# Performance work log

Hardware: AMD Instinct MI355X
Metric: run time of the kernel (lower is better)

The kernel has to match this reference:

```python
import jax, jax.numpy as jnp
import numpy as np
from jax.scipy.linalg import solve_triangular

LOAD = 1e-5       # diagonal loading used by solve_loaded / GEVD stabilization
EPS_DENOM = 1e-6  # clamp in compute_mvdr_bf
REF_MIC = 0


def _covariances(masks, X):
    # masks: (B, S, 3, F, N) real, X: (B, C, F, N) complex
    # returns three (B, S, F, C, C) Hermitian covariance stacks
    return [jnp.einsum('bsfn,bcfn,bdfn->bsfcd', masks[:, :, i], X, jnp.conj(X))
            for i in range(3)]


def _gevd_rtf(A, B):
    # Generalized eigh A v = lam B v via Cholesky whitening; take eigvec of
    # largest eigenvalue, normalize by reference mic (compute_mvdr_rtf_eigh).
    d = A.shape[-1]
    eye = jnp.eye(d, dtype=A.dtype)
    L = jnp.linalg.cholesky(B + LOAD * eye)          # (..., C, C) lower
    T = solve_triangular(L, A, lower=True)           # L^{-1} A
    C = solve_triangular(L, jnp.conj(jnp.swapaxes(T, -1, -2)), lower=True)
    C = jnp.conj(jnp.swapaxes(C, -1, -2))            # L^{-1} A L^{-H}
    C = 0.5 * (C + jnp.conj(jnp.swapaxes(C, -1, -2)))  # enforce Hermitian
    _, u = jnp.linalg.eigh(C)                        # ascending eigenvalues
    u_max = u[..., :, -1]                            # dominant whitened eigvec
    Lh = jnp.conj(jnp.swapaxes(L, -1, -2))
    v = solve_triangular(Lh, u_max[..., None], lower=False)[..., 0]  # L^{-H} u
    return v / v[..., REF_MIC:REF_MIC + 1]


def _mvdr_weights(R_noise, rtf):
    # compute_mvdr_bf: a = (R + load*I)^{-1} rtf ; w = a / max(re(rtf^H a), eps)
    d = R_noise.shape[-1]
    eye = jnp.eye(d, dtype=R_noise.dtype)
    a = jnp.linalg.solve(R_noise + LOAD * eye, rtf[..., None])[..., 0]
    denom = jnp.real(jnp.einsum('...c,...c->...', jnp.conj(rtf), a))
    denom = jnp.maximum(denom, EPS_DENOM)
    return a / denom[..., None]


def setup_inputs() -> dict:
    key = jax.random.key(0)
    k1, k2, k3 = jax.random.split(key, 3)
    B, S, C, F, N = 4, 2, 6, 512, 2000
    return {
        'X_re': jax.random.normal(k1, (B, C, F, N), jnp.float32),
        'X_im': jax.random.normal(k2, (B, C, F, N), jnp.float32),
        'masks': jax.random.uniform(k3, (B, S, 3, F, N), jnp.float32),
    }


def reference(X_re, X_im, masks):
    X = jax.lax.complex(X_re, X_im)                  # (B, C, F, N)
    R_tgt, R_noise_1, R_noise_2 = _covariances(masks, X)
    rtf = _gevd_rtf(R_tgt, R_noise_2)                # (B, S, F, C)
    bf = _mvdr_weights(R_noise_1, rtf)               # (B, S, F, C)
    Y = jnp.einsum('bcfn,bsfc->bsfn', X, jnp.conj(bf))
    # return real/imag stacked to keep harness dtypes real
    return jnp.stack((Y.real, Y.imag), axis=-1)      # (B, S, F, N, 2)
```

## Files before the change

### kernel.cpp

```cpp
#include <hip/hip_runtime.h>

#define B_ 4
#define S_ 2
#define C_ 6
#define F_ 512
#define N_ 2000
#define CH_ (F_ * N_)
#define LOAD_CONST 1e-5
#define EPS_DENOM_ 1e-6
#define NV4 (N_ / 4)
#define NCHUNK 8

__device__ __forceinline__ void gld_lds16(const void* gp, void* lp) {
  __builtin_amdgcn_global_load_lds(
      (const __attribute__((address_space(1))) unsigned int*)gp,
      (__attribute__((address_space(3))) unsigned int*)lp, 16, 0, 0);
}

__global__ __launch_bounds__(64, 2) void cov_kernel(
    const float* __restrict__ Xre, const float* __restrict__ Xim,
    const float* __restrict__ masks, float* __restrict__ cov) {
  __shared__ float sh[2][14][256];

  const int nwg = B_ * F_ * 3;
  const int cpx = nwg / 8;
  const int Bh = blockIdx.x;
  const int l = (Bh & 7) * cpx + (Bh >> 3);
  const int bf = l / 3;
  const int i = l - bf * 3;
  const int b = bf / F_;
  const int f = bf - b * F_;
  const int lane = threadIdx.x;

  const size_t xb = (size_t)b * C_ * CH_ + (size_t)f * N_;

  const float4* gbase[14];
#pragma unroll
  for (int st = 0; st < 12; ++st) {
    const float* p = (st < 6) ? (Xre + xb + (size_t)st * CH_)
                              : (Xim + xb + (size_t)(st - 6) * CH_);
    gbase[st] = (const float4*)p;
  }
  gbase[12] = (const float4*)(masks + ((size_t)b * 6 + i) * CH_ + (size_t)f * N_);
  gbase[13] = (const float4*)(masks + ((size_t)b * 6 + 3 + i) * CH_ + (size_t)f * N_);

  auto stage = [&](int bb, int ch) {
    int idx = ch * 64 + lane;
    if (idx >= NV4) idx = NV4 - 1;
#pragma unroll
    for (int st = 0; st < 14; ++st)
      gld_lds16(gbase[st] + idx, &sh[bb][st][0]);
  };

  float acc0d[6] = {}, acc0r[15] = {}, acc0i[15] = {};
  float acc1d[6] = {}, acc1r[15] = {}, acc1i[15] = {};

  stage(0, 0);
  stage(1, 1);

  for (int ch = 0; ch < NCHUNK; ++ch) {
    const int bb = ch & 1;

    if (ch < NCHUNK - 1) {
      asm volatile("s_waitcnt vmcnt(14)" ::: "memory");
    } else {
      asm volatile("s_waitcnt vmcnt(0)" ::: "memory");
    }

#pragma unroll
    for (int e = 0; e < 4; ++e) {
      const int fo = lane + 64 * e;
      float xre[6], xie[6];
#pragma unroll
      for (int c = 0; c < 6; ++c) {
        xre[c] = sh[bb][c][fo];
        xie[c] = sh[bb][6 + c][fo];
      }
      float m0 = sh[bb][12][fo];
      float m1 = sh[bb][13][fo];
      if (ch * 256 + fo >= N_) { m0 = 0.f; m1 = 0.f; }

#pragma unroll
      for (int c = 0; c < 6; ++c) {
        const float d = fmaf(xre[c], xre[c], xie[c] * xie[c]);
        acc0d[c] = fmaf(m0, d, acc0d[c]);
        acc1d[c] = fmaf(m1, d, acc1d[c]);
      }
      int p = 0;
#pragma unroll
      for (int c = 0; c < 6; ++c) {
#pragma unroll
        for (int d2 = c + 1; d2 < 6; ++d2) {
          const float pr = fmaf(xre[c], xre[d2], xie[c] * xie[d2]);
          const float pi = fmaf(xie[c], xre[d2], -(xre[c] * xie[d2]));
          acc0r[p] = fmaf(m0, pr, acc0r[p]);
          acc0i[p] = fmaf(m0, pi, acc0i[p]);
          acc1r[p] = fmaf(m1, pr, acc1r[p]);
          acc1i[p] = fmaf(m1, pi, acc1i[p]);
          ++p;
        }
      }
    }

    asm volatile("s_waitcnt lgkmcnt(0)" ::: "memory");
    if (ch + 2 < NCHUNK) stage(bb, ch + 2);
  }

#pragma unroll
  for (int c = 0; c < 6; ++c) {
#pragma unroll
    for (int o = 32; o > 0; o >>= 1) {
      acc0d[c] += __shfl_xor(acc0d[c], o, 64);
      acc1d[c] += __shfl_xor(acc1d[c], o, 64);
    }
  }
#pragma unroll
  for (int p2 = 0; p2 < 15; ++p2) {
#pragma unroll
    for (int o = 32; o > 0; o >>= 1) {
      acc0r[p2] += __shfl_xor(acc0r[p2], o, 64);
      acc0i[p2] += __shfl_xor(acc0i[p2], o, 64);
      acc1r[p2] += __shfl_xor(acc1r[p2], o, 64);
      acc1i[p2] += __shfl_xor(acc1i[p2], o, 64);
    }
  }

  if (lane == 0) {
    float* o0 = cov + ((size_t)bf * 6 + i) * 36;
    float* o1 = cov + ((size_t)bf * 6 + 3 + i) * 36;
#pragma unroll
    for (int c = 0; c < 6; ++c) { o0[c] = acc0d[c]; o1[c] = acc1d[c]; }
#pragma unroll
    for (int p2 = 0; p2 < 15; ++p2) {
      o0[6 + 2 * p2] = acc0r[p2];  o0[7 + 2 * p2] = acc0i[p2];
      o1[6 + 2 * p2] = acc1r[p2];  o1[7 + 2 * p2] = acc1i[p2];
    }
  }
}

__device__ __forceinline__ void load_herm(const float* __restrict__ p,
                                          double* mr, double* mi) {
#pragma unroll
  for (int c = 0; c < 6; ++c) { mr[c * 6 + c] = (double)p[c]; mi[c * 6 + c] = 0.0; }
#pragma unroll
  for (int c = 0; c < 6; ++c) {
#pragma unroll
    for (int d = c + 1; d < 6; ++d) {
      const int pidx = 6 + 2 * ((11 - c) * c / 2 + (d - c - 1));
      double re = (double)p[pidx];
      double im = (double)p[pidx + 1];
      mr[c * 6 + d] = re;  mi[c * 6 + d] = im;
      mr[d * 6 + c] = re;  mi[d * 6 + c] = -im;
    }
  }
}

__device__ __forceinline__ void chol6(double* mr, double* mi) {
#pragma unroll
  for (int k = 0; k < 6; ++k) {
    double d = mr[k * 6 + k];
#pragma unroll
    for (int j = 0; j < 6; ++j) {
      if (j < k) d -= mr[k * 6 + j] * mr[k * 6 + j] + mi[k * 6 + j] * mi[k * 6 + j];
    }
    d = sqrt(fmax(d, 1e-300));
    mr[k * 6 + k] = d;  mi[k * 6 + k] = 0.0;
    double inv = 1.0 / d;
#pragma unroll
    for (int r = k + 1; r < 6; ++r) {
      double xre = mr[r * 6 + k], xim = mi[r * 6 + k];
#pragma unroll
      for (int j = 0; j < 6; ++j) {
        if (j < k) {
          double ar = mr[r * 6 + j], ai = mi[r * 6 + j];
          double br = mr[k * 6 + j], bi = mi[k * 6 + j];
          xre -= ar * br + ai * bi;
          xim -= ai * br - ar * bi;
        }
      }
      mr[r * 6 + k] = xre * inv;  mi[r * 6 + k] = xim * inv;
    }
  }
}

__device__ __forceinline__ void chol_solve(const double* mr, const double* mi,
                                           double* xr, double* xi) {
  double yr[6], yi[6];
#pragma unroll
  for (int r = 0; r < 6; ++r) {
    double tr = xr[r], ti = xi[r];
#pragma unroll
    for (int k = 0; k < 6; ++k) {
      if (k < r) {
        double ar = mr[r * 6 + k], ai = mi[r * 6 + k];
        tr -= ar * yr[k] - ai * yi[k];
        ti -= ar * yi[k] + ai * yr[k];
      }
    }
    double inv = 1.0 / mr[r * 6 + r];
    yr[r] = tr * inv;  yi[r] = ti * inv;
  }
#pragma unroll
  for (int r = 5; r >= 0; --r) {
    double tr = yr[r], ti = yi[r];
#pragma unroll
    for (int k = 5; k >= 0; --k) {
      if (k > r) {
        double ar = mr[k * 6 + r], ai = -mi[k * 6 + r];
        tr -= ar * xr[k] - ai * xi[k];
        ti -= ar * xi[k] + ai * xr[k];
      }
    }
    double inv = 1.0 / mr[r * 6 + r];
    xr[r] = tr * inv;  xi[r] = ti * inv;
  }
}

__global__ __launch_bounds__(64, 1) void solve_kernel(
    const float* __restrict__ cov, float* __restrict__ wts) {
  const int t = blockIdx.x * 64 + threadIdx.x;
  if (t >= B_ * S_ * F_) return;
  const int f = t % F_;
  const int s = (t / F_) % S_;
  const int b = t / (F_ * S_);
  const float* cb = cov + (((size_t)(b * F_ + f)) * 6 + s * 3) * 36;

  double Lr[36], Li[36];
  load_herm(cb + 72, Lr, Li);
#pragma unroll
  for (int k = 0; k < 6; ++k) Lr[k * 6 + k] += LOAD_CONST;
  chol6(Lr, Li);

  double Ar[36], Ai[36];
  load_herm(cb, Ar, Ai);

  double Cr[36], Ci[36];
#pragma unroll
  for (int k = 0; k < 36; ++k) { Cr[k] = 0.0; Ci[k] = 0.0; }
#pragma unroll
  for (int j = 0; j < 6; ++j) {
    double yr[6], yi[6];
#pragma unroll
    for (int r = 5; r >= 0; --r) {
      double tr = (r == j) ? 1.0 : 0.0, ti = 0.0;
#pragma unroll
      for (int k = 5; k >= 0; --k) {
        if (k > r) {
          double ar = Lr[k * 6 + r], ai = -Li[k * 6 + r];
          tr -= ar * yr[k] - ai * yi[k];
          ti -= ar * yi[k] + ai * yr[k];
        }
      }
      double inv = 1.0 / Lr[r * 6 + r];
      yr[r] = tr * inv;  yi[r] = ti * inv;
    }
    double zr[6], zi[6];
#pragma unroll
    for (int r = 0; r < 6; ++r) {
      double tr = 0, ti = 0;
#pragma unroll
      for (int k = 0; k < 6; ++k) {
        double ar = Ar[r * 6 + k], ai = Ai[r * 6 + k];
        tr += ar * yr[k] - ai * yi[k];
        ti += ar * yi[k] + ai * yr[k];
      }
      zr[r] = tr;  zi[r] = ti;
    }
    double cr[6], ci2[6];
#pragma unroll
    for (int r = 0; r < 6; ++r) {
      double tr = zr[r], ti = zi[r];
#pragma unroll
      for (int k = 0; k < 6; ++k) {
        if (k < r) {
          double ar = Lr[r * 6 + k], ai = Li[r * 6 + k];
          tr -= ar * cr[k] - ai * ci2[k];
          ti -= ar * ci2[k] + ai * cr[k];
        }
      }
      double inv = 1.0 / Lr[r * 6 + r];
      cr[r] = tr * inv;  ci2[r] = ti * inv;
    }
#pragma unroll
    for (int r = 0; r < 6; ++r) {
      if (r < j)       { Cr[r * 6 + j] += 0.5 * cr[r];  Ci[r * 6 + j] += 0.5 * ci2[r]; }
      else if (r == j) { Cr[r * 6 + r] += cr[r]; }
      else             { Cr[j * 6 + r] += 0.5 * cr[r];  Ci[j * 6 + r] -= 0.5 * ci2[r]; }
    }
  }

  double Gr[36], Gi[36];
#pragma unroll
  for (int k = 0; k < 36; ++k) { Gr[k] = Cr[k]; Gi[k] = Ci[k]; }

#pragma unroll
  for (int sweep = 0; sweep < 8; ++sweep) {
#pragma unroll
    for (int p = 0; p < 5; ++p) {
#pragma unroll
      for (int q = p + 1; q < 6; ++q) {
        double gr = Cr[p * 6 + q], gi = Ci[p * 6 + q];
        double g2 = gr * gr + gi * gi;
        if (g2 > 1e-26) {
          double g = sqrt(g2);
          double wr = gr / g, wi = -gi / g;
          double alpha = Cr[p * 6 + p], beta = Cr[q * 6 + q];
          double tau = (beta - alpha) / (2.0 * g);
          double tt = (tau >= 0.0 ? 1.0 : -1.0) / (fabs(tau) + sqrt(1.0 + tau * tau));
          double cc = 1.0 / sqrt(1.0 + tt * tt);
          double ss = tt * cc;
#pragma unroll
          for (int r = 0; r < 6; ++r) {
            if (r == p || r == q) continue;
            double rpr = (r < p) ? Cr[r * 6 + p] : Cr[p * 6 + r];
            double rpi = (r < p) ? Ci[r * 6 + p] : -Ci[p * 6 + r];
            double rqr = (r < q) ? Cr[r * 6 + q] : Cr[q * 6 + r];
            double rqi = (r < q) ? Ci[r * 6 + q] : -Ci[q * 6 + r];
            double wqr = wr * rqr - wi * rqi;
            double wqi = wr * rqi + wi * rqr;
            double nrpr = cc * rpr - ss * wqr;
            double nrpi = cc * rpi - ss * wqi;
            double nrqr = ss * rpr + cc * wqr;
            double nrqi = ss * rpi + cc * wqi;
            if (r < p) { Cr[r * 6 + p] = nrpr;  Ci[r * 6 + p] = nrpi; }
            else       { Cr[p * 6 + r] = nrpr;  Ci[p * 6 + r] = -nrpi; }
            if (r < q) { Cr[r * 6 + q] = nrqr;  Ci[r * 6 + q] = nrqi; }
            else       { Cr[q * 6 + r] = nrqr;  Ci[q * 6 + r] = -nrqi; }
          }
          Cr[p * 6 + p] = alpha - tt * g;
          Cr[q * 6 + q] = beta + tt * g;
          Cr[p * 6 + q] = 0.0;  Ci[p * 6 + q] = 0.0;
        }
      }
    }
  }

  double lmax = Cr[0];
  lmax = fmax(lmax, Cr[7]);  lmax = fmax(lmax, Cr[14]);
  lmax = fmax(lmax, Cr[21]); lmax = fmax(lmax, Cr[28]);
  lmax = fmax(lmax, Cr[35]);

  double Mr[36], Mi[36];
  double shift = lmax + fmax(1e-8 * fabs(lmax), 1e-30);
#pragma unroll
  for (int r = 0; r < 6; ++r) {
#pragma unroll
    for (int c = 0; c < 6; ++c) {
      double gre, gim;
      if (r == c)     { gre = Gr[r * 6 + c]; gim = 0.0; }
      else if (r < c) { gre = Gr[r * 6 + c]; gim = Gi[r * 6 + c]; }
      else            { gre = Gr[c * 6 + r]; gim = -Gi[c * 6 + r]; }
      Mr[r * 6 + c] = (r == c) ? (shift - gre) : -gre;
      Mi[r * 6 + c] = -gim;
    }
  }
  chol6(Mr, Mi);

  double ur[6] = {1.0, 0.8, -0.6, 1.1, -0.3, 0.5};
  double ui[6] = {0.2, -0.9, 0.7, 0.1, 1.0, -0.4};
#pragma unroll
  for (int it = 0; it < 2; ++it) {
    chol_solve(Mr, Mi, ur, ui);
    double nn = 0;
#pragma unroll
    for (int r = 0; r < 6; ++r) nn += ur[r] * ur[r] + ui[r] * ui[r];
    double innv = 1.0 / sqrt(fmax(nn, 1e-300));
#pragma unroll
    for (int r = 0; r < 6; ++r) { ur[r] *= innv; ui[r] *= innv; }
  }

  double vr[6], vi[6];
#pragma unroll
  for (int r = 5; r >= 0; --r) {
    double tr = ur[r], ti = ui[r];
#pragma unroll
    for (int k = 5; k >= 0; --k) {
      if (k > r) {
        double ar = Lr[k * 6 + r], ai = -Li[k * 6 + r];
        tr -= ar * vr[k] - ai * vi[k];
        ti -= ar * vi[k] + ai * vr[k];
      }
    }
    double inv = 1.0 / Lr[r * 6 + r];
    vr[r] = tr * inv;  vi[r] = ti * inv;
  }

  double id2 = 1.0 / (vr[0] * vr[0] + vi[0] * vi[0]);
  double rtr[6], rti[6];
#pragma unroll
  for (int r = 0; r < 6; ++r) {
    rtr[r] = (vr[r] * vr[0] + vi[r] * vi[0]) * id2;
    rti[r] = (vi[r] * vr[0] - vr[r] * vi[0]) * id2;
  }

  load_herm(cb + 36, Mr, Mi);
#pragma unroll
  for (int k = 0; k < 6; ++k) Mr[k * 6 + k] += LOAD_CONST;
  chol6(Mr, Mi);
  double ar2[6], ai2[6];
#pragma unroll
  for (int r = 0; r < 6; ++r) { ar2[r] = rtr[r]; ai2[r] = rti[r]; }
  chol_solve(Mr, Mi, ar2, ai2);

  double denom = 0;
#pragma unroll
  for (int r = 0; r < 6; ++r) denom += rtr[r] * ar2[r] + rti[r] * ai2[r];
  denom = fmax(denom, EPS_DENOM_);
  double idn = 1.0 / denom;

  float* wp = wts + (size_t)t * 12;
#pragma unroll
  for (int c = 0; c < 6; ++c) {
    wp[2 * c]     = (float)(ar2[c] * idn);
    wp[2 * c + 1] = (float)(-ai2[c] * idn);
  }
}

__global__ __launch_bounds__(256) void bf_kernel(
    const float* __restrict__ Xre, const float* __restrict__ Xim,
    const float* __restrict__ wts, float* __restrict__ out) {
  const int blk = blockIdx.x;
  const int b = blk / F_;
  const int f = blk - b * F_;
  const size_t xb = (size_t)b * C_ * CH_ + (size_t)f * N_;

  float wr[2][6], wi[2][6];
#pragma unroll
  for (int s = 0; s < 2; ++s) {
    const float* wp = wts + (((size_t)(b * S_ + s)) * F_ + f) * 12;
#pragma unroll
    for (int c = 0; c < 6; ++c) { wr[s][c] = wp[2 * c]; wi[s][c] = wp[2 * c + 1]; }
  }
  float4* o0 = (float4*)(out + ((size_t)(b * S_ + 0) * F_ + f) * N_ * 2);
  float4* o1 = (float4*)(out + ((size_t)(b * S_ + 1) * F_ + f) * N_ * 2);

  const int NV = N_ / 4;
  for (int n4 = threadIdx.x; n4 < NV; n4 += 256) {
    float4 xr[6], xi[6];
#pragma unroll
    for (int c = 0; c < 6; ++c) {
      xr[c] = ((const float4*)(Xre + xb + (size_t)c * CH_))[n4];
      xi[c] = ((const float4*)(Xim + xb + (size_t)c * CH_))[n4];
    }
#pragma unroll
    for (int s = 0; s < 2; ++s) {
      float yrx = 0.f, yix = 0.f, yry = 0.f, yiy = 0.f;
      float yrz = 0.f, yiz = 0.f, yrw = 0.f, yiw = 0.f;
#pragma unroll
      for (int c = 0; c < 6; ++c) {
        const float WR = wr[s][c], WI = wi[s][c];
        yrx = fmaf(xr[c].x, WR, fmaf(-xi[c].x, WI, yrx));
        yix = fmaf(xr[c].x, WI, fmaf(xi[c].x, WR, yix));
        yry = fmaf(xr[c].y, WR, fmaf(-xi[c].y, WI, yry));
        yiy = fmaf(xr[c].y, WI, fmaf(xi[c].y, WR, yiy));
        yrz = fmaf(xr[c].z, WR, fmaf(-xi[c].z, WI, yrz));
        yiz = fmaf(xr[c].z, WI, fmaf(xi[c].z, WR, yiz));
        yrw = fmaf(xr[c].w, WR, fmaf(-xi[c].w, WI, yrw));
        yiw = fmaf(xr[c].w, WI, fmaf(xi[c].w, WR, yiw));
      }
      float4* op = s ? o1 : o0;
      op[2 * n4]     = make_float4(yrx, yix, yry, yiy);
      op[2 * n4 + 1] = make_float4(yrz, yiz, yrw, yiw);
    }
  }
}

extern "C" void kernel_launch(void* const* d_in, const int* in_sizes, int n_in,
                              void* d_out, int out_size, void* d_ws, size_t ws_size,
                              hipStream_t stream) {
  const float* Xre   = (const float*)d_in[0];
  const float* Xim   = (const float*)d_in[1];
  const float* masks = (const float*)d_in[2];
  float* out = (float*)d_out;

  float* cov = (float*)d_ws;
  float* wts = cov + (size_t)B_ * F_ * 6 * 36;

  cov_kernel<<<B_ * F_ * 3, 64, 0, stream>>>(Xre, Xim, masks, cov);
  solve_kernel<<<(B_ * S_ * F_ + 63) / 64, 64, 0, stream>>>(cov, wts);
  bf_kernel<<<B_ * F_, 256, 0, stream>>>(Xre, Xim, wts, out);
}
```

Measured before the change: 218.1 us.

## Replace LDS double-buffered async staging with direct float2 register loads in cov kernel

The covariance kernel drops the global_load_lds double-buffered LDS pipeline and instead has each lane load float2 values of X and masks straight into registers, iterating 16 steps. Without LDS, launch bounds move from 2 to 4 waves per SIMD, so more wavefronts can hide memory latency. The trade-off is losing the explicit prefetch overlap and using narrower 8-byte loads, so latency hiding now depends on occupancy and compiler scheduling, and register pressure may be tighter.

```diff
diff --git a/kernel.cpp b/kernel.cpp
--- a/kernel.cpp
+++ b/kernel.cpp
@@ -8,20 +8,11 @@
 #define CH_ (F_ * N_)
 #define LOAD_CONST 1e-5
 #define EPS_DENOM_ 1e-6
-#define NV4 (N_ / 4)
-#define NCHUNK 8
-
-__device__ __forceinline__ void gld_lds16(const void* gp, void* lp) {
-  __builtin_amdgcn_global_load_lds(
-      (const __attribute__((address_space(1))) unsigned int*)gp,
-      (__attribute__((address_space(3))) unsigned int*)lp, 16, 0, 0);
-}
-
-__global__ __launch_bounds__(64, 2) void cov_kernel(
+#define NV2 (N_ / 2)
+
+__global__ __launch_bounds__(64, 4) void cov_kernel(
     const float* __restrict__ Xre, const float* __restrict__ Xim,
     const float* __restrict__ masks, float* __restrict__ cov) {
-  __shared__ float sh[2][14][256];
-
   const int nwg = B_ * F_ * 3;
   const int cpx = nwg / 8;
   const int Bh = blockIdx.x;
@@ -34,57 +25,51 @@
 
   const size_t xb = (size_t)b * C_ * CH_ + (size_t)f * N_;
 
-  const float4* gbase[14];
-#pragma unroll
-  for (int st = 0; st < 12; ++st) {
-    const float* p = (st < 6) ? (Xre + xb + (size_t)st * CH_)
-                              : (Xim + xb + (size_t)(st - 6) * CH_);
-    gbase[st] = (const float4*)p;
-  }
-  gbase[12] = (const float4*)(masks + ((size_t)b * 6 + i) * CH_ + (size_t)f * N_);
-  gbase[13] = (const float4*)(masks + ((size_t)b * 6 + 3 + i) * CH_ + (size_t)f * N_);
-
-  auto stage = [&](int bb, int ch) {
-    int idx = ch * 64 + lane;
-    if (idx >= NV4) idx = NV4 - 1;
-#pragma unroll
-    for (int st = 0; st < 14; ++st)
-      gld_lds16(gbase[st] + idx, &sh[bb][st][0]);
-  };
+  const float2* xrp[6];
+  const float2* xip[6];
+#pragma unroll
+  for (int c = 0; c < 6; ++c) {
+    xrp[c] = (const float2*)(Xre + xb + (size_t)c * CH_);
+    xip[c] = (const float2*)(Xim + xb + (size_t)c * CH_);
+  }
+  const float2* mp0 =
+      (const float2*)(masks + ((size_t)b * 6 + i) * CH_ + (size_t)f * N_);
+  const float2* mp1 =
+      (const float2*)(masks + ((size_t)b * 6 + 3 + i) * CH_ + (size_t)f * N_);
 
   float acc0d[6] = {}, acc0r[15] = {}, acc0i[15] = {};
   float acc1d[6] = {}, acc1r[15] = {}, acc1i[15] = {};
 
-  stage(0, 0);
-  stage(1, 1);
-
-  for (int ch = 0; ch < NCHUNK; ++ch) {
-    const int bb = ch & 1;
-
-    if (ch < NCHUNK - 1) {
-      asm volatile("s_waitcnt vmcnt(14)" ::: "memory");
-    } else {
-      asm volatile("s_waitcnt vmcnt(0)" ::: "memory");
-    }
-
-#pragma unroll
-    for (int e = 0; e < 4; ++e) {
-      const int fo = lane + 64 * e;
+  for (int it = 0; it < 16; ++it) {
+    const int idx = lane + it * 64;
+    const int a = (idx < NV2) ? idx : (NV2 - 1);
+
+    float2 m0 = mp0[a];
+    float2 m1 = mp1[a];
+    float2 xr[6], xi[6];
+#pragma unroll
+    for (int c = 0; c < 6; ++c) {
+      xr[c] = xrp[c][a];
+      xi[c] = xip[c][a];
+    }
+    if (idx >= NV2) { m0 = make_float2(0.f, 0.f); m1 = make_float2(0.f, 0.f); }
+
+#pragma unroll
+    for (int e = 0; e < 2; ++e) {
       float xre[6], xie[6];
 #pragma unroll
       for (int c = 0; c < 6; ++c) {
-        xre[c] = sh[bb][c][fo];
-        xie[c] = sh[bb][6 + c][fo];
-      }
-      float m0 = sh[bb][12][fo];
-      float m1 = sh[bb][13][fo];
-      if (ch * 256 + fo >= N_) { m0 = 0.f; m1 = 0.f; }
+        xre[c] = e ? xr[c].y : xr[c].x;
+        xie[c] = e ? xi[c].y : xi[c].x;
+      }
+      const float mm0 = e ? m0.y : m0.x;
+      const float mm1 = e ? m1.y : m1.x;
 
 #pragma unroll
       for (int c = 0; c < 6; ++c) {
         const float d = fmaf(xre[c], xre[c], xie[c] * xie[c]);
-        acc0d[c] = fmaf(m0, d, acc0d[c]);
-        acc1d[c] = fmaf(m1, d, acc1d[c]);
+        acc0d[c] = fmaf(mm0, d, acc0d[c]);
+        acc1d[c] = fmaf(mm1, d, acc1d[c]);
       }
       int p = 0;
 #pragma unroll
@@ -93,17 +78,14 @@
         for (int d2 = c + 1; d2 < 6; ++d2) {
           const float pr = fmaf(xre[c], xre[d2], xie[c] * xie[d2]);
           const float pi = fmaf(xie[c], xre[d2], -(xre[c] * xie[d2]));
-          acc0r[p] = fmaf(m0, pr, acc0r[p]);
-          acc0i[p] = fmaf(m0, pi, acc0i[p]);
-          acc1r[p] = fmaf(m1, pr, acc1r[p]);
-          acc1i[p] = fmaf(m1, pi, acc1i[p]);
+          acc0r[p] = fmaf(mm0, pr, acc0r[p]);
+          acc0i[p] = fmaf(mm0, pi, acc0i[p]);
+          acc1r[p] = fmaf(mm1, pr, acc1r[p]);
+          acc1i[p] = fmaf(mm1, pi, acc1i[p]);
           ++p;
         }
       }
     }
-
-    asm volatile("s_waitcnt lgkmcnt(0)" ::: "memory");
-    if (ch + 2 < NCHUNK) stage(bb, ch + 2);
   }
 
 #pragma unroll
```

Measured after the change: 345.3 us. 1.58x slower.
